# Kernel optimization log

Hardware: AMD Instinct MI355X
Metric: run time of the kernel (lower is better)

## Reference

```python
import jax, jax.numpy as jnp
import numpy as np

NORMAL_WEIGHT = 0.001
B, C, N = 8, 6, 4096  # N == n_samples, so no subsampling branch


def setup_inputs() -> dict:
    key = jax.random.key(0)
    k1, k2 = jax.random.split(key)
    a = jax.random.normal(k1, (B, C, N), dtype=jnp.float32)
    b = jax.random.normal(k2, (B, C, N), dtype=jnp.float32)
    return {"a": a, "b": b}


def _chamfer_with_normals(a, b):
    # a, b: [B, 6, N] -> [B, N, 6]
    at = jnp.swapaxes(a, 1, 2)
    bt = jnp.swapaxes(b, 1, 2)
    ap, an = at[:, :, 0:3], at[:, :, 3:6]  # points / normals [B,N,3]
    bp, bn = bt[:, :, 0:3], bt[:, :, 3:6]
    # batch pairwise squared distances: pd[b,i,j] = ||ap_i - bp_j||^2
    aa = jnp.sum(ap * ap, axis=-1)  # [B,N]
    bb = jnp.sum(bp * bp, axis=-1)  # [B,N]
    ab = jnp.einsum('bic,bjc->bij', ap, bp)  # [B,N,N]
    pd = aa[:, :, None] + bb[:, None, :] - 2.0 * ab
    # Faithful to torch: mma[b,i,j]=a_normals[j], mmb[b,i,j]=b_normals[i]
    # so d_norm[b,i,j] = 1 - dot(b_normals[i], a_normals[j])
    d_norm = 1.0 - jnp.einsum('bic,bjc->bij', bn, an)  # [B,N,N]
    d = pd + NORMAL_WEIGHT * d_norm
    chamfer_sym = jnp.sum(jnp.min(d, axis=2)) + jnp.sum(jnp.min(d, axis=1))
    return chamfer_sym / a.shape[0]


def reference(a, b):
    return _chamfer_with_normals(a, b)
```

## Files before the change

### kernel.cpp

```cpp
#include <hip/hip_runtime.h>


constexpr int   NPTS  = 4096;
constexpr int   CPB   = 6;
constexpr int   BATCH = 8;
constexpr float W     = 0.001f;

typedef _Float16 f16x8 __attribute__((ext_vector_type(8)));
typedef float    f32x4 __attribute__((ext_vector_type(4)));

#define MFMA32(A_, B_, C_) __builtin_amdgcn_mfma_f32_16x16x32_f16((A_), (B_), (C_), 0, 0, 0)

__device__ inline void fsplit(float x, _Float16& h, _Float16& l) {
    h = (_Float16)x;
    l = (_Float16)(x - (float)h);
}

__global__ __launch_bounds__(256) void prep_kernel(
    const float* __restrict__ A, const float* __restrict__ B,
    _Float16* __restrict__ rowT, _Float16* __restrict__ colpack,
    float* __restrict__ out)
{
    const int g = blockIdx.x * 256 + threadIdx.x;
    if (g == 0) out[0] = 0.f;
    const int j = g & (NPTS - 1), bd = g >> 12, dir = bd >> 3, batch = bd & 7;
    const int bb = batch * CPB * NPTS;
    const float* rowPos = dir ? B : A;
    const float* rowNrm = dir ? A : B;
    const float* colPos = dir ? A : B;
    const float* colNrm = dir ? B : A;

    const float p0 = rowPos[bb + 0*NPTS + j], p1 = rowPos[bb + 1*NPTS + j],
                p2 = rowPos[bb + 2*NPTS + j];
    const float rn0 = rowNrm[bb + 3*NPTS + j], rn1 = rowNrm[bb + 4*NPTS + j],
                rn2 = rowNrm[bb + 5*NPTS + j];
    const float r6[6] = {-2.f*p0, -2.f*p1, -2.f*p2, -W*rn0, -W*rn1, -W*rn2};
    const float aa = fmaf(p0, p0, fmaf(p1, p1, p2*p2));
    _Float16 rh[6], rl[6], ah, al;
#pragma unroll
    for (int c = 0; c < 6; ++c) fsplit(r6[c], rh[c], rl[c]);
    fsplit(aa, ah, al);
    const _Float16 one = (_Float16)1.f, zz = (_Float16)0.f;
    f16x8 r0 = {rh[0], rh[1], rh[2], rh[3], rh[4], rh[5], rl[0], rl[1]};
    f16x8 r1 = {rl[2], rl[3], rl[4], rl[5], one, ah, al, zz};
    *(f16x8*)(rowT + (size_t)g * 16)     = r0;
    *(f16x8*)(rowT + (size_t)g * 16 + 8) = r1;

    const float q0 = colPos[bb + 0*NPTS + j], q1 = colPos[bb + 1*NPTS + j],
                q2 = colPos[bb + 2*NPTS + j];
    const float cn0 = colNrm[bb + 3*NPTS + j], cn1 = colNrm[bb + 4*NPTS + j],
                cn2 = colNrm[bb + 5*NPTS + j];
    const float c6[6] = {q0, q1, q2, cn0, cn1, cn2};
    const float bias = fmaf(q0, q0, fmaf(q1, q1, q2*q2)) + W;
    _Float16 ch[6], cl[6], bh, bl;
#pragma unroll
    for (int c = 0; c < 6; ++c) fsplit(c6[c], ch[c], cl[c]);
    fsplit(bias, bh, bl);
    f16x8 v0 = {ch[0], ch[1], ch[2], ch[3], ch[4], ch[5], ch[0], ch[1]};
    f16x8 v1 = {ch[2], ch[3], ch[4], ch[5], cl[0], cl[1], cl[2], cl[3]};
    f16x8 v2 = {cl[4], cl[5], cl[0], cl[1], cl[2], cl[3], cl[4], cl[5]};
    f16x8 v3 = {bh, bl, one, one, zz, zz, zz, zz};
    _Float16* cp = colpack + (size_t)g * 32;
    *(f16x8*)(cp)      = v0;
    *(f16x8*)(cp + 8)  = v1;
    *(f16x8*)(cp + 16) = v2;
    *(f16x8*)(cp + 24) = v3;
}

__global__ __launch_bounds__(256, 2) void chamfer_mfma_kernel(
    const _Float16* __restrict__ rowT, const _Float16* __restrict__ colpack,
    float* __restrict__ partial)
{
    const int dir = blockIdx.z, batch = blockIdx.y, bd = dir * BATCH + batch;
    const int rg = blockIdx.x >> 2, s = blockIdx.x & 3;
    const int tid = threadIdx.x, w = tid >> 6, lane = tid & 63;
    const int quad = lane >> 4, l16 = lane & 15;

    __shared__ _Float16 lds[512 * 32];

    f16x8 a[8];
    {
        const _Float16* rb = rowT + ((size_t)bd * NPTS + rg * 512) * 16;
#pragma unroll
        for (int rt = 0; rt < 8; ++rt) {
            const int row = (w * 8 + rt) * 16 + l16;
            const f16x8 rec0 = *(const f16x8*)(rb + (size_t)row * 16);
            const f16x8 rec1 = *(const f16x8*)(rb + (size_t)row * 16 + 8);
            f16x8 af;
            if (quad == 0)      af = rec0;
            else if (quad == 1) af = f16x8{rec1[0], rec1[1], rec1[2], rec1[3],
                                           rec0[0], rec0[1], rec0[2], rec0[3]};
            else if (quad == 2) af = f16x8{rec0[4], rec0[5], rec0[6], rec0[7],
                                           rec1[0], rec1[1], rec1[2], rec1[3]};
            else                af = f16x8{rec1[4], rec1[4], rec1[5], rec1[6],
                                           (_Float16)0.f, (_Float16)0.f,
                                           (_Float16)0.f, (_Float16)0.f};
            a[rt] = af;
        }
    }

    float m[8][4];
#pragma unroll
    for (int rt = 0; rt < 8; ++rt)
#pragma unroll
        for (int r_ = 0; r_ < 4; ++r_) m[rt][r_] = 3.4e38f;

    const _Float16* cpb = colpack + ((size_t)bd * NPTS + s * 1024) * 32;
    const f32x4 z = {0.f, 0.f, 0.f, 0.f};

    for (int ph = 0; ph < 2; ++ph) {
        if (ph) __syncthreads();
        {
            const uint4* src = (const uint4*)(cpb + (size_t)ph * 512 * 32);
            uint4* dst = (uint4*)lds;
#pragma unroll
            for (int i = 0; i < 8; ++i) dst[tid + i * 256] = src[tid + i * 256];
        }
        __syncthreads();
        for (int ct = 0; ct < 32; ct += 2) {
            const f16x8 b0 = *(const f16x8*)&lds[(ct * 16 + l16) * 32 + quad * 8];
            const f16x8 b1 = *(const f16x8*)&lds[((ct + 1) * 16 + l16) * 32 + quad * 8];
#pragma unroll
            for (int rt = 0; rt < 8; ++rt) {
                f32x4 acc0 = MFMA32(a[rt], b0, z);
                f32x4 acc1 = MFMA32(a[rt], b1, z);
#pragma unroll
                for (int r_ = 0; r_ < 4; ++r_)
                    m[rt][r_] = fminf(m[rt][r_], fminf(acc0[r_], acc1[r_]));
            }
        }
    }

#pragma unroll
    for (int rt = 0; rt < 8; ++rt)
#pragma unroll
        for (int r_ = 0; r_ < 4; ++r_) {
            float v = m[rt][r_];
            v = fminf(v, __shfl_xor(v, 1));
            v = fminf(v, __shfl_xor(v, 2));
            v = fminf(v, __shfl_xor(v, 4));
            v = fminf(v, __shfl_xor(v, 8));
            m[rt][r_] = v;
        }
    if (l16 == 0) {
        float* pb = partial + ((size_t)(s * 16 + bd)) * NPTS + rg * 512;
#pragma unroll
        for (int rt = 0; rt < 8; ++rt) {
            const int rb_ = (w * 8 + rt) * 16 + quad * 4;
            *(float4*)(pb + rb_) = make_float4(m[rt][0], m[rt][1], m[rt][2], m[rt][3]);
        }
    }
}

__global__ __launch_bounds__(256) void reduce_kernel(
    const float* __restrict__ partial, float* __restrict__ out)
{
    const int g = blockIdx.x * 256 + threadIdx.x;
    const int bd = g >> 12, row = g & (NPTS - 1);
    float v = partial[(size_t)(0 * 16 + bd) * NPTS + row];
    v = fminf(v, partial[(size_t)(1 * 16 + bd) * NPTS + row]);
    v = fminf(v, partial[(size_t)(2 * 16 + bd) * NPTS + row]);
    v = fminf(v, partial[(size_t)(3 * 16 + bd) * NPTS + row]);
    for (int off = 32; off; off >>= 1)
        v += __shfl_down(v, off, 64);
    __shared__ float sred[4];
    if ((threadIdx.x & 63) == 0) sred[threadIdx.x >> 6] = v;
    __syncthreads();
    if (threadIdx.x == 0)
        atomicAdd(out, (sred[0] + sred[1] + sred[2] + sred[3]) * 0.125f);
}

extern "C" void kernel_launch(void* const* d_in, const int* in_sizes, int n_in,
                              void* d_out, int out_size, void* d_ws, size_t ws_size,
                              hipStream_t stream) {
    const float* A = (const float*)d_in[0];
    const float* B = (const float*)d_in[1];
    float* out = (float*)d_out;

    _Float16* rowT    = (_Float16*)d_ws;
    _Float16* colpack = rowT + (size_t)2 * BATCH * NPTS * 16;
    float*    partial = (float*)((char*)d_ws + (size_t)6 * 1024 * 1024);

    prep_kernel<<<dim3(2 * BATCH * NPTS / 256), 256, 0, stream>>>(A, B, rowT, colpack, out);
    chamfer_mfma_kernel<<<dim3(32, BATCH, 2), 256, 0, stream>>>(rowT, colpack, partial);
    reduce_kernel<<<dim3(2 * BATCH * NPTS / 256), 256, 0, stream>>>(partial, out);
}
```

Before: 88.08 us.

## Fuse fp16 split-packing prep into the MFMA chamfer kernel

Removes the separate prep kernel: each block now reads the raw fp32 point and normal data, does the hi/lo fp16 split and packing for its own 1024 columns directly into LDS, and builds its row fragments in registers. The column layout in LDS changes to four quad-major planes, so all 1024 columns sit in LDS at once and the two-phase reload with its extra barrier goes away. This saves one launch and the global round trip of the packed buffers. In exchange, the split and pack work is repeated across the blocks that share the same data, and LDS use per block doubles to 64 KB, which may limit occupancy.

```diff
diff --git a/kernel.cpp b/kernel.cpp
--- a/kernel.cpp
+++ b/kernel.cpp
@@ -16,87 +16,70 @@
     l = (_Float16)(x - (float)h);
 }
 
-__global__ __launch_bounds__(256) void prep_kernel(
+__global__ __launch_bounds__(256, 2) void chamfer_fused_kernel(
     const float* __restrict__ A, const float* __restrict__ B,
-    _Float16* __restrict__ rowT, _Float16* __restrict__ colpack,
-    float* __restrict__ out)
-{
-    const int g = blockIdx.x * 256 + threadIdx.x;
-    if (g == 0) out[0] = 0.f;
-    const int j = g & (NPTS - 1), bd = g >> 12, dir = bd >> 3, batch = bd & 7;
-    const int bb = batch * CPB * NPTS;
-    const float* rowPos = dir ? B : A;
-    const float* rowNrm = dir ? A : B;
-    const float* colPos = dir ? A : B;
-    const float* colNrm = dir ? B : A;
-
-    const float p0 = rowPos[bb + 0*NPTS + j], p1 = rowPos[bb + 1*NPTS + j],
-                p2 = rowPos[bb + 2*NPTS + j];
-    const float rn0 = rowNrm[bb + 3*NPTS + j], rn1 = rowNrm[bb + 4*NPTS + j],
-                rn2 = rowNrm[bb + 5*NPTS + j];
-    const float r6[6] = {-2.f*p0, -2.f*p1, -2.f*p2, -W*rn0, -W*rn1, -W*rn2};
-    const float aa = fmaf(p0, p0, fmaf(p1, p1, p2*p2));
-    _Float16 rh[6], rl[6], ah, al;
-#pragma unroll
-    for (int c = 0; c < 6; ++c) fsplit(r6[c], rh[c], rl[c]);
-    fsplit(aa, ah, al);
-    const _Float16 one = (_Float16)1.f, zz = (_Float16)0.f;
-    f16x8 r0 = {rh[0], rh[1], rh[2], rh[3], rh[4], rh[5], rl[0], rl[1]};
-    f16x8 r1 = {rl[2], rl[3], rl[4], rl[5], one, ah, al, zz};
-    *(f16x8*)(rowT + (size_t)g * 16)     = r0;
-    *(f16x8*)(rowT + (size_t)g * 16 + 8) = r1;
-
-    const float q0 = colPos[bb + 0*NPTS + j], q1 = colPos[bb + 1*NPTS + j],
-                q2 = colPos[bb + 2*NPTS + j];
-    const float cn0 = colNrm[bb + 3*NPTS + j], cn1 = colNrm[bb + 4*NPTS + j],
-                cn2 = colNrm[bb + 5*NPTS + j];
-    const float c6[6] = {q0, q1, q2, cn0, cn1, cn2};
-    const float bias = fmaf(q0, q0, fmaf(q1, q1, q2*q2)) + W;
-    _Float16 ch[6], cl[6], bh, bl;
-#pragma unroll
-    for (int c = 0; c < 6; ++c) fsplit(c6[c], ch[c], cl[c]);
-    fsplit(bias, bh, bl);
-    f16x8 v0 = {ch[0], ch[1], ch[2], ch[3], ch[4], ch[5], ch[0], ch[1]};
-    f16x8 v1 = {ch[2], ch[3], ch[4], ch[5], cl[0], cl[1], cl[2], cl[3]};
-    f16x8 v2 = {cl[4], cl[5], cl[0], cl[1], cl[2], cl[3], cl[4], cl[5]};
-    f16x8 v3 = {bh, bl, one, one, zz, zz, zz, zz};
-    _Float16* cp = colpack + (size_t)g * 32;
-    *(f16x8*)(cp)      = v0;
-    *(f16x8*)(cp + 8)  = v1;
-    *(f16x8*)(cp + 16) = v2;
-    *(f16x8*)(cp + 24) = v3;
-}
-
-__global__ __launch_bounds__(256, 2) void chamfer_mfma_kernel(
-    const _Float16* __restrict__ rowT, const _Float16* __restrict__ colpack,
-    float* __restrict__ partial)
+    float* __restrict__ partial, float* __restrict__ out)
 {
     const int dir = blockIdx.z, batch = blockIdx.y, bd = dir * BATCH + batch;
     const int rg = blockIdx.x >> 2, s = blockIdx.x & 3;
     const int tid = threadIdx.x, w = tid >> 6, lane = tid & 63;
     const int quad = lane >> 4, l16 = lane & 15;
+    const float* rowPos = dir ? B : A;
+    const float* rowNrm = dir ? A : B;
+    const float* colPos = dir ? A : B;
+    const float* colNrm = dir ? B : A;
+    const int bb = batch * CPB * NPTS;
+    const _Float16 one = (_Float16)1.f, zz = (_Float16)0.f;
 
-    __shared__ _Float16 lds[512 * 32];
+    if (blockIdx.x == 0 && blockIdx.y == 0 && blockIdx.z == 0 && tid == 0)
+        out[0] = 0.f;
+
+    __shared__ alignas(16) _Float16 lds[4 * 1024 * 8];
+
+#pragma unroll
+    for (int p = 0; p < 4; ++p) {
+        const int j  = p * 256 + tid;
+        const int cj = s * 1024 + j;
+        const float q0 = colPos[bb + 0*NPTS + cj], q1 = colPos[bb + 1*NPTS + cj],
+                    q2 = colPos[bb + 2*NPTS + cj];
+        const float n0 = colNrm[bb + 3*NPTS + cj], n1 = colNrm[bb + 4*NPTS + cj],
+                    n2 = colNrm[bb + 5*NPTS + cj];
+        const float c6[6] = {q0, q1, q2, n0, n1, n2};
+        const float bias = fmaf(q0, q0, fmaf(q1, q1, q2*q2)) + W;
+        _Float16 ch[6], cl[6], bh, bl;
+#pragma unroll
+        for (int c = 0; c < 6; ++c) fsplit(c6[c], ch[c], cl[c]);
+        fsplit(bias, bh, bl);
+        f16x8 v0 = {ch[0], ch[1], ch[2], ch[3], ch[4], ch[5], ch[0], ch[1]};
+        f16x8 v1 = {ch[2], ch[3], ch[4], ch[5], cl[0], cl[1], cl[2], cl[3]};
+        f16x8 v2 = {cl[4], cl[5], cl[0], cl[1], cl[2], cl[3], cl[4], cl[5]};
+        f16x8 v3 = {bh, bl, one, one, zz, zz, zz, zz};
+        *(f16x8*)&lds[0 * 8192 + j * 8] = v0;
+        *(f16x8*)&lds[1 * 8192 + j * 8] = v1;
+        *(f16x8*)&lds[2 * 8192 + j * 8] = v2;
+        *(f16x8*)&lds[3 * 8192 + j * 8] = v3;
+    }
 
     f16x8 a[8];
-    {
-        const _Float16* rb = rowT + ((size_t)bd * NPTS + rg * 512) * 16;
 #pragma unroll
-        for (int rt = 0; rt < 8; ++rt) {
-            const int row = (w * 8 + rt) * 16 + l16;
-            const f16x8 rec0 = *(const f16x8*)(rb + (size_t)row * 16);
-            const f16x8 rec1 = *(const f16x8*)(rb + (size_t)row * 16 + 8);
-            f16x8 af;
-            if (quad == 0)      af = rec0;
-            else if (quad == 1) af = f16x8{rec1[0], rec1[1], rec1[2], rec1[3],
-                                           rec0[0], rec0[1], rec0[2], rec0[3]};
-            else if (quad == 2) af = f16x8{rec0[4], rec0[5], rec0[6], rec0[7],
-                                           rec1[0], rec1[1], rec1[2], rec1[3]};
-            else                af = f16x8{rec1[4], rec1[4], rec1[5], rec1[6],
-                                           (_Float16)0.f, (_Float16)0.f,
-                                           (_Float16)0.f, (_Float16)0.f};
-            a[rt] = af;
-        }
+    for (int rt = 0; rt < 8; ++rt) {
+        const int row = rg * 512 + (w * 8 + rt) * 16 + l16;
+        const float p0 = rowPos[bb + 0*NPTS + row], p1 = rowPos[bb + 1*NPTS + row],
+                    p2 = rowPos[bb + 2*NPTS + row];
+        const float rn0 = rowNrm[bb + 3*NPTS + row], rn1 = rowNrm[bb + 4*NPTS + row],
+                    rn2 = rowNrm[bb + 5*NPTS + row];
+        const float r6[6] = {-2.f*p0, -2.f*p1, -2.f*p2, -W*rn0, -W*rn1, -W*rn2};
+        const float aa = fmaf(p0, p0, fmaf(p1, p1, p2*p2));
+        _Float16 rh[6], rl[6], ah, al;
+#pragma unroll
+        for (int c = 0; c < 6; ++c) fsplit(r6[c], rh[c], rl[c]);
+        fsplit(aa, ah, al);
+        f16x8 af;
+        if (quad == 0)      af = f16x8{rh[0], rh[1], rh[2], rh[3], rh[4], rh[5], rl[0], rl[1]};
+        else if (quad == 1) af = f16x8{rl[2], rl[3], rl[4], rl[5], rh[0], rh[1], rh[2], rh[3]};
+        else if (quad == 2) af = f16x8{rh[4], rh[5], rl[0], rl[1], rl[2], rl[3], rl[4], rl[5]};
+        else                af = f16x8{one, one, ah, al, zz, zz, zz, zz};
+        a[rt] = af;
     }
 
     float m[8][4];
@@ -105,29 +88,20 @@
 #pragma unroll
         for (int r_ = 0; r_ < 4; ++r_) m[rt][r_] = 3.4e38f;
 
-    const _Float16* cpb = colpack + ((size_t)bd * NPTS + s * 1024) * 32;
+    __syncthreads();
+
+    const _Float16* lq = &lds[quad * 8192];
     const f32x4 z = {0.f, 0.f, 0.f, 0.f};
-
-    for (int ph = 0; ph < 2; ++ph) {
-        if (ph) __syncthreads();
-        {
-            const uint4* src = (const uint4*)(cpb + (size_t)ph * 512 * 32);
-            uint4* dst = (uint4*)lds;
+    for (int ct = 0; ct < 64; ct += 2) {
+        const f16x8 b0 = *(const f16x8*)&lq[(ct * 16 + l16) * 8];
+        const f16x8 b1 = *(const f16x8*)&lq[((ct + 1) * 16 + l16) * 8];
 #pragma unroll
-            for (int i = 0; i < 8; ++i) dst[tid + i * 256] = src[tid + i * 256];
-        }
-        __syncthreads();
-        for (int ct = 0; ct < 32; ct += 2) {
-            const f16x8 b0 = *(const f16x8*)&lds[(ct * 16 + l16) * 32 + quad * 8];
-            const f16x8 b1 = *(const f16x8*)&lds[((ct + 1) * 16 + l16) * 32 + quad * 8];
+        for (int rt = 0; rt < 8; ++rt) {
+            f32x4 acc0 = MFMA32(a[rt], b0, z);
+            f32x4 acc1 = MFMA32(a[rt], b1, z);
 #pragma unroll
-            for (int rt = 0; rt < 8; ++rt) {
-                f32x4 acc0 = MFMA32(a[rt], b0, z);
-                f32x4 acc1 = MFMA32(a[rt], b1, z);
-#pragma unroll
-                for (int r_ = 0; r_ < 4; ++r_)
-                    m[rt][r_] = fminf(m[rt][r_], fminf(acc0[r_], acc1[r_]));
-            }
+            for (int r_ = 0; r_ < 4; ++r_)
+                m[rt][r_] = fminf(m[rt][r_], fminf(acc0[r_], acc1[r_]));
         }
     }
 
@@ -175,13 +149,9 @@
                               hipStream_t stream) {
     const float* A = (const float*)d_in[0];
     const float* B = (const float*)d_in[1];
-    float* out = (float*)d_out;
+    float* out     = (float*)d_out;
+    float* partial = (float*)d_ws;
 
-    _Float16* rowT    = (_Float16*)d_ws;
-    _Float16* colpack = rowT + (size_t)2 * BATCH * NPTS * 16;
-    float*    partial = (float*)((char*)d_ws + (size_t)6 * 1024 * 1024);
-
-    prep_kernel<<<dim3(2 * BATCH * NPTS / 256), 256, 0, stream>>>(A, B, rowT, colpack, out);
-    chamfer_mfma_kernel<<<dim3(32, BATCH, 2), 256, 0, stream>>>(rowT, colpack, partial);
+    chamfer_fused_kernel<<<dim3(32, BATCH, 2), 256, 0, stream>>>(A, B, partial, out);
     reduce_kernel<<<dim3(2 * BATCH * NPTS / 256), 256, 0, stream>>>(partial, out);
 }
```

Measured after the change: 77.13 us. 1.14x faster.
